# Optimization experiments

Hardware: AMD Instinct MI355X
Metric: run time of the kernel (lower is better)

Reference implementation:

```python
import jax, jax.numpy as jnp
import numpy as np

N, E = 50000, 800000
D_IN, D_H, D_OUT = 128, 256, 128
EPS = 1e-5  # BatchNorm eps


def _glorot(key, fan_in, fan_out):
    s = jnp.sqrt(6.0 / (fan_in + fan_out))
    return jax.random.uniform(key, (fan_in, fan_out), jnp.float32, -s, s)


def setup_inputs() -> dict:
    key = jax.random.key(0)
    ks = jax.random.split(key, 8)
    x = jax.random.normal(ks[0], (N, D_IN), jnp.float32)
    edge_index = jax.random.randint(ks[1], (2, E), 0, N, dtype=jnp.int64)
    return {
        "x": x,
        "edge_index": edge_index,
        # GCNConv layer 0: input_dim -> hidden
        "W0": _glorot(ks[2], D_IN, D_H), "b0": jnp.zeros((D_H,), jnp.float32),
        "g0": jnp.ones((D_H,), jnp.float32), "be0": jnp.zeros((D_H,), jnp.float32),
        # GCNConv layer 1: hidden -> hidden (residual middle layer)
        "W1": _glorot(ks[3], D_H, D_H), "b1": jnp.zeros((D_H,), jnp.float32),
        "g1": jnp.ones((D_H,), jnp.float32), "be1": jnp.zeros((D_H,), jnp.float32),
        # GCNConv layer 2: hidden -> output
        "W2": _glorot(ks[4], D_H, D_OUT), "b2": jnp.zeros((D_OUT,), jnp.float32),
    }


def reference(x, edge_index, W0, b0, g0, be0, W1, b1, g1, be1, W2, b2):
    n = x.shape[0]
    loop = jnp.arange(n, dtype=edge_index.dtype)
    src = jnp.concatenate([edge_index[0], loop])  # add self loops
    dst = jnp.concatenate([edge_index[1], loop])
    # symmetric GCN normalization: deg computed over destinations (self loops weight 1)
    deg = jax.ops.segment_sum(jnp.ones_like(src, x.dtype), dst, num_segments=n)
    dinv = jnp.where(deg > 0, jax.lax.rsqrt(deg), 0.0)
    norm = dinv[src] * dinv[dst]  # [E+N]

    def conv(h, W, b):
        m = h @ W                              # [N, F_out] transform first (F_out small)
        m = m[src] * norm[:, None]             # gather + edge scale
        return jax.ops.segment_sum(m, dst, num_segments=n) + b

    def bn(h, g, be):  # training-mode batch stats over the node dim
        mu = h.mean(axis=0)
        var = h.var(axis=0)
        return (h - mu) * jax.lax.rsqrt(var + EPS) * g + be

    # layer 0
    h = jax.nn.relu(bn(conv(x, W0, b0), g0, be0))
    # middle residual layer
    h = jax.nn.relu(bn(conv(h, W1, b1), g1, be1)) + h
    # output layer + input residual (input_dim == output_dim, no projection)
    h = conv(h, W2, b2)
    return h + x
```

## Files before the change

kernel.cpp:

```cpp
#include <hip/hip_runtime.h>

#define BN_EPS 1e-5f

static constexpr int D_IN = 128;

using u16 = unsigned short;
using f32x4  = __attribute__((ext_vector_type(4))) float;
using bf16x8 = __attribute__((ext_vector_type(8))) __bf16;

union FragU { uint4 u; bf16x8 v; };

__device__ __forceinline__ u16 f2bf(float f) {
  unsigned int u = __float_as_uint(f);
  u += 0x7FFFu + ((u >> 16) & 1u);
  return (u16)(u >> 16);
}
__device__ __forceinline__ float bf2f(u16 h) {
  return __uint_as_float(((unsigned int)h) << 16);
}


__global__ __launch_bounds__(256) void count_kernel(const int* __restrict__ dst, int E,
                                                    int* __restrict__ cnt) {
  int e = blockIdx.x * 256 + threadIdx.x;
  if (e < E) atomicAdd(&cnt[dst[e]], 1);
}

__global__ __launch_bounds__(1024) void scan_sum_kernel(const int* __restrict__ cnt, int n,
                                                        int* __restrict__ bsum,
                                                        float* __restrict__ dinv) {
  __shared__ int sdata[1024];
  int i = blockIdx.x * 1024 + threadIdx.x;
  int v = (i < n) ? cnt[i] : 0;
  if (i < n) dinv[i] = rsqrtf((float)v + 1.0f);
  sdata[threadIdx.x] = v;
  __syncthreads();
  for (int s = 512; s > 0; s >>= 1) {
    if (threadIdx.x < s) sdata[threadIdx.x] += sdata[threadIdx.x + s];
    __syncthreads();
  }
  if (threadIdx.x == 0) bsum[blockIdx.x] = sdata[0];
}

__global__ __launch_bounds__(1024) void scan_final_kernel(const int* __restrict__ cnt, int n,
                                                          const int* __restrict__ bsum,
                                                          int* __restrict__ rowptr) {
  __shared__ int wt[16];
  __shared__ int sboff;
  int i = blockIdx.x * 1024 + threadIdx.x;
  int lane = threadIdx.x & 63, w = threadIdx.x >> 6;
  int v = (i < n) ? cnt[i] : 0;
  int x = v;
  #pragma unroll
  for (int d = 1; d < 64; d <<= 1) {
    int t = __shfl_up(x, d, 64);
    if (lane >= d) x += t;
  }
  if (lane == 63) wt[w] = x;
  __syncthreads();
  if (threadIdx.x == 0) {
    int run = 0;
    #pragma unroll
    for (int k = 0; k < 16; ++k) { int t = wt[k]; wt[k] = run; run += t; }
    int bo = 0;
    for (int b = 0; b < blockIdx.x; ++b) bo += bsum[b];
    sboff = bo;
  }
  __syncthreads();
  if (i < n) {
    rowptr[i] = x - v + wt[w] + sboff;
    if (i == n - 1) rowptr[n] = x + wt[w] + sboff;
  }
}

__global__ __launch_bounds__(256) void fill_kernel(const int* __restrict__ src,
                                                   const int* __restrict__ dst, int E,
                                                   const int* __restrict__ rowptr,
                                                   int* __restrict__ cursor, int* __restrict__ col) {
  int e = blockIdx.x * 256 + threadIdx.x;
  if (e < E) {
    int d = dst[e];
    int p = atomicAdd(&cursor[d], 1);
    col[rowptr[d] + p] = src[e];
  }
}


__global__ __launch_bounds__(256) void prep_kernel(int* __restrict__ zbuf, int nz, int BZ,
                                                   const float* __restrict__ x, u16* __restrict__ x_bf,
                                                   const float* __restrict__ W0, u16* __restrict__ Wt0,
                                                   const float* __restrict__ W1, u16* __restrict__ Wt1,
                                                   const float* __restrict__ W2, u16* __restrict__ Wt2,
                                                   int N, int BX) {
  int b = blockIdx.x, tid = threadIdx.x;
  if (b < BZ) {
    int i = b * 256 + tid;
    if (i < nz) zbuf[i] = 0;
  } else if (b < BZ + BX) {
    int i = (b - BZ) * 256 + tid;
    if (i < N * 32) {
      float4 v = ((const float4*)x)[i];
      u16 o[4] = { f2bf(v.x), f2bf(v.y), f2bf(v.z), f2bf(v.w) };
      ((uint2*)x_bf)[i] = *(uint2*)o;
    }
  } else if (b < BZ + BX + 128) {
    int idx = (b - BZ - BX) * 256 + tid;
    int k = idx >> 8, nc = idx & 255;
    Wt0[nc * 128 + k] = f2bf(W0[idx]);
  } else if (b < BZ + BX + 384) {
    int idx = (b - BZ - BX - 128) * 256 + tid;
    int k = idx >> 8, nc = idx & 255;
    Wt1[nc * 256 + k] = f2bf(W1[idx]);
  } else {
    int idx = (b - BZ - BX - 384) * 256 + tid;
    int k = idx >> 7, nc = idx & 127;
    Wt2[nc * 256 + k] = f2bf(W2[idx]);
  }
}


template<int F, bool BIAS, bool FINAL>
__global__ __launch_bounds__(256) void agg_bf16(const u16* __restrict__ in,
                                                const int* __restrict__ rowptr,
                                                const int* __restrict__ col,
                                                const float* __restrict__ dinv,
                                                const float* __restrict__ bias,
                                                const float* __restrict__ xres,
                                                void* __restrict__ outv, int n) {
  constexpr int V = F / 64;
  int node = blockIdx.x * 4 + (threadIdx.x >> 6);
  if (node >= n) return;
  int lane = threadIdx.x & 63;
  const int off = lane * V;
  const size_t rowbase = (size_t)node * F + off;

  float di = dinv[node];
  float acc[V];
  {
    u16 t[V];
    if constexpr (V == 4) *(uint2*)t = *(const uint2*)(in + rowbase);
    else                  *(unsigned int*)t = *(const unsigned int*)(in + rowbase);
    #pragma unroll
    for (int j = 0; j < V; ++j) acc[j] = di * bf2f(t[j]);
  }

  int e   = __builtin_amdgcn_readfirstlane(rowptr[node]);
  int end = __builtin_amdgcn_readfirstlane(rowptr[node + 1]);
  for (; e + 4 <= end; e += 4) {
    int s0 = col[e], s1 = col[e + 1], s2 = col[e + 2], s3 = col[e + 3];
    float w0 = dinv[s0], w1 = dinv[s1], w2 = dinv[s2], w3 = dinv[s3];
    u16 t0[V], t1[V], t2[V], t3[V];
    if constexpr (V == 4) {
      *(uint2*)t0 = *(const uint2*)(in + (size_t)s0 * F + off);
      *(uint2*)t1 = *(const uint2*)(in + (size_t)s1 * F + off);
      *(uint2*)t2 = *(const uint2*)(in + (size_t)s2 * F + off);
      *(uint2*)t3 = *(const uint2*)(in + (size_t)s3 * F + off);
    } else {
      *(unsigned int*)t0 = *(const unsigned int*)(in + (size_t)s0 * F + off);
      *(unsigned int*)t1 = *(const unsigned int*)(in + (size_t)s1 * F + off);
      *(unsigned int*)t2 = *(const unsigned int*)(in + (size_t)s2 * F + off);
      *(unsigned int*)t3 = *(const unsigned int*)(in + (size_t)s3 * F + off);
    }
    #pragma unroll
    for (int j = 0; j < V; ++j) acc[j] = fmaf(w0, bf2f(t0[j]), acc[j]);
    #pragma unroll
    for (int j = 0; j < V; ++j) acc[j] = fmaf(w1, bf2f(t1[j]), acc[j]);
    #pragma unroll
    for (int j = 0; j < V; ++j) acc[j] = fmaf(w2, bf2f(t2[j]), acc[j]);
    #pragma unroll
    for (int j = 0; j < V; ++j) acc[j] = fmaf(w3, bf2f(t3[j]), acc[j]);
  }
  for (; e < end; ++e) {
    int s0 = col[e];
    float w0 = dinv[s0];
    u16 t0[V];
    if constexpr (V == 4) *(uint2*)t0 = *(const uint2*)(in + (size_t)s0 * F + off);
    else                  *(unsigned int*)t0 = *(const unsigned int*)(in + (size_t)s0 * F + off);
    #pragma unroll
    for (int j = 0; j < V; ++j) acc[j] = fmaf(w0, bf2f(t0[j]), acc[j]);
  }

  #pragma unroll
  for (int j = 0; j < V; ++j) acc[j] *= di;
  if constexpr (BIAS) {
    #pragma unroll
    for (int j = 0; j < V; ++j) acc[j] += bias[off + j];
  }
  if constexpr (FINAL) {
    float* out = (float*)outv;
    float xr[V];
    if constexpr (V == 2) *(float2*)xr = *(const float2*)(xres + rowbase);
    else                  *(float4*)xr = *(const float4*)(xres + rowbase);
    #pragma unroll
    for (int j = 0; j < V; ++j) acc[j] += xr[j];
    if constexpr (V == 2) *(float2*)(out + rowbase) = *(float2*)acc;
    else                  *(float4*)(out + rowbase) = *(float4*)acc;
  } else {
    u16* out = (u16*)outv;
    u16 o[V];
    #pragma unroll
    for (int j = 0; j < V; ++j) o[j] = f2bf(acc[j]);
    if constexpr (V == 4) *(uint2*)(out + rowbase) = *(uint2*)o;
    else                  *(unsigned int*)(out + rowbase) = *(unsigned int*)o;
  }
}


template<int K, int NN, bool BIAS, bool STATS>
__global__ __launch_bounds__(256, 2) void gemm_stream(const u16* __restrict__ A,
                                                      const u16* __restrict__ Wt,
                                                      const float* __restrict__ bias,
                                                      u16* __restrict__ C,
                                                      float* __restrict__ partial, int M) {
  constexpr int CPR = K / 8;
  __shared__ u16 Blds[128 * K];
  __shared__ float sstat[256];
  const int tid = threadIdx.x;
  const int lane = tid & 63;
  const int wid = tid >> 6;
  const int bn = blockIdx.y * 128;
  const int kh = lane >> 4;

  if constexpr (STATS) { sstat[tid] = 0.f; }

  const u16* Bsrc = Wt + (size_t)bn * K;
  #pragma unroll
  for (int i = 0; i < CPR / 2; ++i) {
    int flat = i * 256 + tid;
    int r = flat / CPR;
    int c = flat & (CPR - 1);
    __builtin_amdgcn_global_load_lds(
        (const __attribute__((address_space(1))) void*)(Bsrc + (size_t)r * K + (c ^ (r & 7)) * 8),
        (__attribute__((address_space(3))) void*)(&Blds[flat * 8]),
        16, 0, 0);
  }
  __syncthreads();

  float cs[8] = {}, cq[8] = {};
  const int nch = (M + 63) / 64;
  for (int ch = blockIdx.x * 4 + wid; ch < nch; ch += gridDim.x * 4) {
    const int r0 = ch * 64;
    const u16* arow[4];
    #pragma unroll
    for (int rf = 0; rf < 4; ++rf) {
      int row = r0 + rf * 16 + (lane & 15);
      if (row >= M) row = M - 1;
      arow[rf] = A + (size_t)row * K + kh * 8;
    }
    f32x4 acc[4][8] = {};
    #pragma unroll
    for (int ks = 0; ks < K / 32; ++ks) {
      FragU a[4], b[8];
      #pragma unroll
      for (int rf = 0; rf < 4; ++rf)
        a[rf].u = *(const uint4*)(arow[rf] + ks * 32);
      #pragma unroll
      for (int cf = 0; cf < 8; ++cf) {
        int rr = cf * 16 + (lane & 15);
        int c = ks * 4 + kh;
        b[cf].u = *(const uint4*)(&Blds[rr * K + ((c ^ (rr & 7)) * 8)]);
      }
      #pragma unroll
      for (int rf = 0; rf < 4; ++rf)
        #pragma unroll
        for (int cf = 0; cf < 8; ++cf)
          acc[rf][cf] = __builtin_amdgcn_mfma_f32_16x16x32_bf16(a[rf].v, b[cf].v,
                                                                acc[rf][cf], 0, 0, 0);
    }
    #pragma unroll
    for (int cf = 0; cf < 8; ++cf) {
      int gc = bn + cf * 16 + (lane & 15);
      float bv = 0.f;
      if constexpr (BIAS) bv = bias[gc];
      #pragma unroll
      for (int rf = 0; rf < 4; ++rf) {
        int gr0 = r0 + rf * 16 + kh * 4;
        #pragma unroll
        for (int j = 0; j < 4; ++j) {
          int gr = gr0 + j;
          if (gr < M) {
            float v = acc[rf][cf][j] + bv;
            C[(size_t)gr * NN + gc] = f2bf(v);
            if constexpr (STATS) { cs[cf] += v; cq[cf] = fmaf(v, v, cq[cf]); }
          }
        }
      }
    }
  }

  if constexpr (STATS) {
    #pragma unroll
    for (int cf = 0; cf < 8; ++cf) {
      float s = cs[cf], q = cq[cf];
      s += __shfl_xor(s, 16, 64); q += __shfl_xor(q, 16, 64);
      s += __shfl_xor(s, 32, 64); q += __shfl_xor(q, 32, 64);
      if (kh == 0) {
        int cl = cf * 16 + (lane & 15);
        atomicAdd(&sstat[cl], s);
        atomicAdd(&sstat[128 + cl], q);
      }
    }
    __syncthreads();
    if (tid < 128) {
      size_t pb = ((size_t)blockIdx.y * gridDim.x + blockIdx.x) * 256;
      partial[pb + tid]       = sstat[tid];
      partial[pb + 128 + tid] = sstat[128 + tid];
    }
  }
}


template<int F>
__global__ __launch_bounds__(256) void stats_bf16(const u16* __restrict__ m, int n,
                                                  float* __restrict__ partial) {
  constexpr int COLS = F / 4;
  constexpr int RG = 256 / COLS;
  int c4 = threadIdx.x % COLS;
  int rg = threadIdx.x / COLS;
  float s[4] = {}, q[4] = {};
  for (int r = blockIdx.x * RG + rg; r < n; r += gridDim.x * RG) {
    u16 t[4];
    *(uint2*)t = *(const uint2*)(m + (size_t)r * F + c4 * 4);
    #pragma unroll
    for (int j = 0; j < 4; ++j) { float v = bf2f(t[j]); s[j] += v; q[j] = fmaf(v, v, q[j]); }
  }
  __shared__ float ls[256][8];
  #pragma unroll
  for (int j = 0; j < 4; ++j) { ls[threadIdx.x][j] = s[j]; ls[threadIdx.x][4 + j] = q[j]; }
  __syncthreads();
  if (rg == 0) {
    for (int g = 1; g < RG; ++g) {
      #pragma unroll
      for (int j = 0; j < 4; ++j) {
        s[j] += ls[g * COLS + c4][j];
        q[j] += ls[g * COLS + c4][4 + j];
      }
    }
    #pragma unroll
    for (int j = 0; j < 4; ++j) {
      partial[(size_t)blockIdx.x * 2 * F + c4 * 4 + j]     = s[j];
      partial[(size_t)blockIdx.x * 2 * F + F + c4 * 4 + j] = q[j];
    }
  }
}

__global__ __launch_bounds__(64) void finalize_gemm(const float* __restrict__ partial, int GX, int n,
                                                    const float* __restrict__ g,
                                                    const float* __restrict__ be,
                                                    float* __restrict__ scale,
                                                    float* __restrict__ shift) {
  int c = blockIdx.x;
  int by = c >> 7, cl = c & 127;
  float s = 0.f, q = 0.f;
  for (int bx = threadIdx.x; bx < GX; bx += 64) {
    const float* pb = partial + ((size_t)by * GX + bx) * 256;
    s += pb[cl]; q += pb[128 + cl];
  }
  #pragma unroll
  for (int d = 32; d > 0; d >>= 1) { s += __shfl_down(s, d, 64); q += __shfl_down(q, d, 64); }
  if (threadIdx.x == 0) {
    float inv_n = 1.0f / (float)n;
    float mu = s * inv_n;
    float var = q * inv_n - mu * mu;
    float rs = rsqrtf(var + BN_EPS);
    float sc = rs * g[c];
    scale[c] = sc;
    shift[c] = fmaf(-mu, sc, be[c]);
  }
}

__global__ __launch_bounds__(64) void finalize_agg(const float* __restrict__ partial, int nb, int n,
                                                   const float* __restrict__ g,
                                                   const float* __restrict__ be,
                                                   float* __restrict__ scale,
                                                   float* __restrict__ shift) {
  int c = blockIdx.x;
  float s = 0.f, q = 0.f;
  for (int b = threadIdx.x; b < nb; b += 64) {
    s += partial[(size_t)b * 512 + c];
    q += partial[(size_t)b * 512 + 256 + c];
  }
  #pragma unroll
  for (int d = 32; d > 0; d >>= 1) { s += __shfl_down(s, d, 64); q += __shfl_down(q, d, 64); }
  if (threadIdx.x == 0) {
    float inv_n = 1.0f / (float)n;
    float mu = s * inv_n;
    float var = q * inv_n - mu * mu;
    float rs = rsqrtf(var + BN_EPS);
    float sc = rs * g[c];
    scale[c] = sc;
    shift[c] = fmaf(-mu, sc, be[c]);
  }
}

template<int F, bool RES>
__global__ __launch_bounds__(256) void apply_bf16(const u16* __restrict__ m,
                                                  const float* __restrict__ scale,
                                                  const float* __restrict__ shift,
                                                  const u16* __restrict__ res,
                                                  u16* __restrict__ out, int n) {
  int i = blockIdx.x * 256 + threadIdx.x;
  if (i >= n * (F / 8)) return;
  int c = i & (F / 8 - 1);
  u16 t[8];
  *(uint4*)t = *(const uint4*)(m + (size_t)i * 8);
  float sc[8], sh[8];
  *(float4*)sc       = ((const float4*)scale)[c * 2];
  *(float4*)(sc + 4) = ((const float4*)scale)[c * 2 + 1];
  *(float4*)sh       = ((const float4*)shift)[c * 2];
  *(float4*)(sh + 4) = ((const float4*)shift)[c * 2 + 1];
  float h[8];
  #pragma unroll
  for (int j = 0; j < 8; ++j) h[j] = fmaxf(fmaf(bf2f(t[j]), sc[j], sh[j]), 0.f);
  if constexpr (RES) {
    u16 r[8];
    *(uint4*)r = *(const uint4*)(res + (size_t)i * 8);
    #pragma unroll
    for (int j = 0; j < 8; ++j) h[j] += bf2f(r[j]);
  }
  u16 o[8];
  #pragma unroll
  for (int j = 0; j < 8; ++j) o[j] = f2bf(h[j]);
  *(uint4*)(out + (size_t)i * 8) = *(uint4*)o;
}


extern "C" void kernel_launch(void* const* d_in, const int* in_sizes, int n_in,
                              void* d_out, int out_size, void* d_ws, size_t ws_size,
                              hipStream_t stream) {
  const float* x   = (const float*)d_in[0];
  const int*   ei  = (const int*)d_in[1];
  const float* W0  = (const float*)d_in[2];
  const float* b0  = (const float*)d_in[3];
  const float* g0  = (const float*)d_in[4];
  const float* be0 = (const float*)d_in[5];
  const float* W1  = (const float*)d_in[6];
  const float* b1  = (const float*)d_in[7];
  const float* g1  = (const float*)d_in[8];
  const float* be1 = (const float*)d_in[9];
  const float* W2  = (const float*)d_in[10];
  const float* b2  = (const float*)d_in[11];
  float* out = (float*)d_out;

  const int N = in_sizes[0] / D_IN;
  const int E = in_sizes[1] / 2;
  const int* esrc = ei;
  const int* edst = ei + E;

  char* p = (char*)d_ws;
  auto alloc = [&](size_t bytes) { char* r = p; p += (bytes + 255) & ~(size_t)255; return r; };
  int* cnt     = (int*)alloc((size_t)2 * N * 4);
  int* cursor  = cnt + N;
  int* rowptr  = (int*)alloc(((size_t)N + 1) * 4);
  int* col     = (int*)alloc((size_t)E * 4);
  float* dinv  = (float*)alloc((size_t)N * 4);
  const int nb = (N + 1023) / 1024;
  int* bsum    = (int*)alloc((size_t)nb * 4);
  constexpr int SB = 128;
  const int GX = 196;
  float* partial = (float*)alloc((size_t)(SB > GX * 2 ? SB : GX * 2) * 512 * 4);
  float* scalev  = (float*)alloc(256 * 4);
  float* shiftv  = (float*)alloc(256 * 4);
  u16* Wt0 = (u16*)alloc((size_t)256 * 128 * 2);
  u16* Wt1 = (u16*)alloc((size_t)256 * 256 * 2);
  u16* Wt2 = (u16*)alloc((size_t)128 * 256 * 2);
  u16* slotX  = (u16*)alloc((size_t)N * 128 * 2);
  u16* slotAM = (u16*)alloc((size_t)N * 256 * 2);
  u16* slotMH = (u16*)alloc((size_t)N * 256 * 2);
  u16* slotAH = (u16*)alloc((size_t)N * 256 * 2);
  u16* x_bf = slotX;  u16* m2 = slotX;
  u16* a0   = slotAM; u16* m1 = slotAM;
  u16* m0   = slotMH; u16* h0 = slotMH;
  u16* a1   = slotAH; u16* h1 = slotAH;
  (void)ws_size; (void)n_in; (void)out_size;

  const int BZ = (2 * N + 255) / 256;
  const int BX = (N * 32 + 255) / 256;
  prep_kernel<<<BZ + BX + 512, 256, 0, stream>>>(cnt, 2 * N, BZ, x, x_bf,
                                                 W0, Wt0, W1, Wt1, W2, Wt2, N, BX);
  count_kernel<<<(E + 255) / 256, 256, 0, stream>>>(edst, E, cnt);
  scan_sum_kernel<<<nb, 1024, 0, stream>>>(cnt, N, bsum, dinv);
  scan_final_kernel<<<nb, 1024, 0, stream>>>(cnt, N, bsum, rowptr);
  fill_kernel<<<(E + 255) / 256, 256, 0, stream>>>(esrc, edst, E, rowptr, cursor, col);

  const int aggGrid = (N + 3) / 4;

  agg_bf16<128, false, false><<<aggGrid, 256, 0, stream>>>(x_bf, rowptr, col, dinv,
                                                           nullptr, nullptr, a0, N);
  gemm_stream<128, 256, true, true><<<dim3(GX, 2), 256, 0, stream>>>(a0, Wt0, b0, m0, partial, N);
  finalize_gemm<<<256, 64, 0, stream>>>(partial, GX, N, g0, be0, scalev, shiftv);
  apply_bf16<256, false><<<(N * 32 + 255) / 256, 256, 0, stream>>>(m0, scalev, shiftv,
                                                                   nullptr, h0, N);

  gemm_stream<256, 256, false, false><<<dim3(GX, 2), 256, 0, stream>>>(h0, Wt1, nullptr, m1,
                                                                       nullptr, N);
  agg_bf16<256, true, false><<<aggGrid, 256, 0, stream>>>(m1, rowptr, col, dinv,
                                                          b1, nullptr, a1, N);
  stats_bf16<256><<<SB, 256, 0, stream>>>(a1, N, partial);
  finalize_agg<<<256, 64, 0, stream>>>(partial, SB, N, g1, be1, scalev, shiftv);
  apply_bf16<256, true><<<(N * 32 + 255) / 256, 256, 0, stream>>>(a1, scalev, shiftv,
                                                                  h0, h1, N);

  gemm_stream<256, 128, false, false><<<dim3(GX, 1), 256, 0, stream>>>(h1, Wt2, nullptr, m2,
                                                                       nullptr, N);
  agg_bf16<128, true, true><<<aggGrid, 256, 0, stream>>>(m2, rowptr, col, dinv,
                                                         b2, x, out, N);
}
```

Baseline: 409.3 us.

## Stage GEMM epilogue through LDS for wide stores; fuse BN finalize via last-block

The GEMM epilogue now writes each row's bf16 outputs into a small per-wave LDS staging buffer and stores 16-byte vectors to global memory, replacing scattered 2-byte stores. The BN stat finalization kernels are removed and folded into the GEMM and stats kernels using an atomic done-counter, so the last block to finish reduces the partials. This cuts two kernel launches and improves store coalescing, at the cost of extra LDS traffic, an LDS round trip per row, and a serial reduction in a single block.

Result: slower. 515.6 us (+26.0%).

```diff
diff --git a/kernel.cpp b/kernel.cpp
--- a/kernel.cpp
+++ b/kernel.cpp
@@ -206,18 +206,26 @@
 }
 
 
-template<int K, int NN, bool BIAS, bool STATS>
+template<int K, int NN, bool BIAS, bool STATS, bool FIN>
 __global__ __launch_bounds__(256, 2) void gemm_stream(const u16* __restrict__ A,
                                                       const u16* __restrict__ Wt,
                                                       const float* __restrict__ bias,
                                                       u16* __restrict__ C,
-                                                      float* __restrict__ partial, int M) {
+                                                      float* __restrict__ partial,
+                                                      int* __restrict__ done,
+                                                      const float* __restrict__ g,
+                                                      const float* __restrict__ be,
+                                                      float* __restrict__ scale,
+                                                      float* __restrict__ shift, int M) {
   constexpr int CPR = K / 8;
   __shared__ u16 Blds[128 * K];
+  __shared__ __align__(16) u16 Cst[4][4][136];
   __shared__ float sstat[256];
+  __shared__ int lastflag;
   const int tid = threadIdx.x;
   const int lane = tid & 63;
   const int wid = tid >> 6;
+  const int l15 = lane & 15;
   const int bn = blockIdx.y * 128;
   const int kh = lane >> 4;
 
@@ -236,6 +244,10 @@
   }
   __syncthreads();
 
+  float bv[8];
+  #pragma unroll
+  for (int cf = 0; cf < 8; ++cf) bv[cf] = BIAS ? bias[bn + cf * 16 + l15] : 0.f;
+
   float cs[8] = {}, cq[8] = {};
   const int nch = (M + 63) / 64;
   for (int ch = blockIdx.x * 4 + wid; ch < nch; ch += gridDim.x * 4) {
@@ -243,7 +255,7 @@
     const u16* arow[4];
     #pragma unroll
     for (int rf = 0; rf < 4; ++rf) {
-      int row = r0 + rf * 16 + (lane & 15);
+      int row = r0 + rf * 16 + l15;
       if (row >= M) row = M - 1;
       arow[rf] = A + (size_t)row * K + kh * 8;
     }
@@ -256,7 +268,7 @@
         a[rf].u = *(const uint4*)(arow[rf] + ks * 32);
       #pragma unroll
       for (int cf = 0; cf < 8; ++cf) {
-        int rr = cf * 16 + (lane & 15);
+        int rr = cf * 16 + l15;
         int c = ks * 4 + kh;
         b[cf].u = *(const uint4*)(&Blds[rr * K + ((c ^ (rr & 7)) * 8)]);
       }
@@ -268,22 +280,19 @@
                                                                 acc[rf][cf], 0, 0, 0);
     }
     #pragma unroll
-    for (int cf = 0; cf < 8; ++cf) {
-      int gc = bn + cf * 16 + (lane & 15);
-      float bv = 0.f;
-      if constexpr (BIAS) bv = bias[gc];
+    for (int rf = 0; rf < 4; ++rf) {
       #pragma unroll
-      for (int rf = 0; rf < 4; ++rf) {
-        int gr0 = r0 + rf * 16 + kh * 4;
+      for (int j = 0; j < 4; ++j) {
+        int grw = r0 + rf * 16 + kh * 4 + j;
         #pragma unroll
-        for (int j = 0; j < 4; ++j) {
-          int gr = gr0 + j;
-          if (gr < M) {
-            float v = acc[rf][cf][j] + bv;
-            C[(size_t)gr * NN + gc] = f2bf(v);
-            if constexpr (STATS) { cs[cf] += v; cq[cf] = fmaf(v, v, cq[cf]); }
-          }
+        for (int cf = 0; cf < 8; ++cf) {
+          float v = acc[rf][cf][j] + bv[cf];
+          if constexpr (STATS) { if (grw < M) { cs[cf] += v; cq[cf] = fmaf(v, v, cq[cf]); } }
+          Cst[wid][kh][cf * 16 + l15] = f2bf(v);
         }
+        int gr = r0 + rf * 16 + kh * 4 + j;
+        uint4 d = *(const uint4*)(&Cst[wid][kh][l15 * 8]);
+        if (gr < M) *(uint4*)(C + (size_t)gr * NN + bn + l15 * 8) = d;
       }
     }
   }
@@ -295,7 +304,7 @@
       s += __shfl_xor(s, 16, 64); q += __shfl_xor(q, 16, 64);
       s += __shfl_xor(s, 32, 64); q += __shfl_xor(q, 32, 64);
       if (kh == 0) {
-        int cl = cf * 16 + (lane & 15);
+        int cl = cf * 16 + l15;
         atomicAdd(&sstat[cl], s);
         atomicAdd(&sstat[128 + cl], q);
       }
@@ -306,15 +315,46 @@
       partial[pb + tid]       = sstat[tid];
       partial[pb + 128 + tid] = sstat[128 + tid];
     }
+    if constexpr (FIN) {
+      __threadfence();
+      if (tid == 0) {
+        int old = atomicAdd(done, 1);
+        lastflag = (old == (int)(gridDim.x * gridDim.y) - 1);
+      }
+      __syncthreads();
+      if (lastflag) {
+        __threadfence();
+        int c = tid;
+        int by = c >> 7, cl = c & 127;
+        float s = 0.f, q = 0.f;
+        for (int bx = 0; bx < (int)gridDim.x; ++bx) {
+          const float* pb = partial + ((size_t)by * gridDim.x + bx) * 256;
+          s += pb[cl]; q += pb[128 + cl];
+        }
+        float inv_n = 1.0f / (float)M;
+        float mu = s * inv_n;
+        float var = q * inv_n - mu * mu;
+        float rs = rsqrtf(var + BN_EPS);
+        float sc = rs * g[c];
+        scale[c] = sc;
+        shift[c] = fmaf(-mu, sc, be[c]);
+      }
+    }
   }
 }
 
 
 template<int F>
 __global__ __launch_bounds__(256) void stats_bf16(const u16* __restrict__ m, int n,
-                                                  float* __restrict__ partial) {
+                                                  float* __restrict__ partial,
+                                                  int* __restrict__ done,
+                                                  const float* __restrict__ g,
+                                                  const float* __restrict__ be,
+                                                  float* __restrict__ scale,
+                                                  float* __restrict__ shift) {
   constexpr int COLS = F / 4;
   constexpr int RG = 256 / COLS;
+  __shared__ int lastflag;
   int c4 = threadIdx.x % COLS;
   int rg = threadIdx.x / COLS;
   float s[4] = {}, q[4] = {};
@@ -329,11 +369,11 @@
   for (int j = 0; j < 4; ++j) { ls[threadIdx.x][j] = s[j]; ls[threadIdx.x][4 + j] = q[j]; }
   __syncthreads();
   if (rg == 0) {
-    for (int g = 1; g < RG; ++g) {
+    for (int gg = 1; gg < RG; ++gg) {
       #pragma unroll
       for (int j = 0; j < 4; ++j) {
-        s[j] += ls[g * COLS + c4][j];
-        q[j] += ls[g * COLS + c4][4 + j];
+        s[j] += ls[gg * COLS + c4][j];
+        q[j] += ls[gg * COLS + c4][4 + j];
       }
     }
     #pragma unroll
@@ -342,50 +382,23 @@
       partial[(size_t)blockIdx.x * 2 * F + F + c4 * 4 + j] = q[j];
     }
   }
-}
-
-__global__ __launch_bounds__(64) void finalize_gemm(const float* __restrict__ partial, int GX, int n,
-                                                    const float* __restrict__ g,
-                                                    const float* __restrict__ be,
-                                                    float* __restrict__ scale,
-                                                    float* __restrict__ shift) {
-  int c = blockIdx.x;
-  int by = c >> 7, cl = c & 127;
-  float s = 0.f, q = 0.f;
-  for (int bx = threadIdx.x; bx < GX; bx += 64) {
-    const float* pb = partial + ((size_t)by * GX + bx) * 256;
-    s += pb[cl]; q += pb[128 + cl];
-  }
-  #pragma unroll
-  for (int d = 32; d > 0; d >>= 1) { s += __shfl_down(s, d, 64); q += __shfl_down(q, d, 64); }
+  __threadfence();
   if (threadIdx.x == 0) {
+    int old = atomicAdd(done, 1);
+    lastflag = (old == (int)gridDim.x - 1);
+  }
+  __syncthreads();
+  if (lastflag) {
+    __threadfence();
+    int c = threadIdx.x;
+    float ss = 0.f, qq = 0.f;
+    for (int b = 0; b < (int)gridDim.x; ++b) {
+      ss += partial[(size_t)b * 2 * F + c];
+      qq += partial[(size_t)b * 2 * F + F + c];
+    }
     float inv_n = 1.0f / (float)n;
-    float mu = s * inv_n;
-    float var = q * inv_n - mu * mu;
-    float rs = rsqrtf(var + BN_EPS);
-    float sc = rs * g[c];
-    scale[c] = sc;
-    shift[c] = fmaf(-mu, sc, be[c]);
-  }
-}
-
-__global__ __launch_bounds__(64) void finalize_agg(const float* __restrict__ partial, int nb, int n,
-                                                   const float* __restrict__ g,
-                                                   const float* __restrict__ be,
-                                                   float* __restrict__ scale,
-                                                   float* __restrict__ shift) {
-  int c = blockIdx.x;
-  float s = 0.f, q = 0.f;
-  for (int b = threadIdx.x; b < nb; b += 64) {
-    s += partial[(size_t)b * 512 + c];
-    q += partial[(size_t)b * 512 + 256 + c];
-  }
-  #pragma unroll
-  for (int d = 32; d > 0; d >>= 1) { s += __shfl_down(s, d, 64); q += __shfl_down(q, d, 64); }
-  if (threadIdx.x == 0) {
-    float inv_n = 1.0f / (float)n;
-    float mu = s * inv_n;
-    float var = q * inv_n - mu * mu;
+    float mu = ss * inv_n;
+    float var = qq * inv_n - mu * mu;
     float rs = rsqrtf(var + BN_EPS);
     float sc = rs * g[c];
     scale[c] = sc;
@@ -449,8 +462,9 @@
 
   char* p = (char*)d_ws;
   auto alloc = [&](size_t bytes) { char* r = p; p += (bytes + 255) & ~(size_t)255; return r; };
-  int* cnt     = (int*)alloc((size_t)2 * N * 4);
+  int* cnt     = (int*)alloc(((size_t)2 * N + 2) * 4);
   int* cursor  = cnt + N;
+  int* done    = cnt + 2 * N;
   int* rowptr  = (int*)alloc(((size_t)N + 1) * 4);
   int* col     = (int*)alloc((size_t)E * 4);
   float* dinv  = (float*)alloc((size_t)N * 4);
@@ -474,9 +488,10 @@
   u16* a1   = slotAH; u16* h1 = slotAH;
   (void)ws_size; (void)n_in; (void)out_size;
 
-  const int BZ = (2 * N + 255) / 256;
+  const int NZ = 2 * N + 2;
+  const int BZ = (NZ + 255) / 256;
   const int BX = (N * 32 + 255) / 256;
-  prep_kernel<<<BZ + BX + 512, 256, 0, stream>>>(cnt, 2 * N, BZ, x, x_bf,
+  prep_kernel<<<BZ + BX + 512, 256, 0, stream>>>(cnt, NZ, BZ, x, x_bf,
                                                  W0, Wt0, W1, Wt1, W2, Wt2, N, BX);
   count_kernel<<<(E + 255) / 256, 256, 0, stream>>>(edst, E, cnt);
   scan_sum_kernel<<<nb, 1024, 0, stream>>>(cnt, N, bsum, dinv);
@@ -487,22 +502,21 @@
 
   agg_bf16<128, false, false><<<aggGrid, 256, 0, stream>>>(x_bf, rowptr, col, dinv,
                                                            nullptr, nullptr, a0, N);
-  gemm_stream<128, 256, true, true><<<dim3(GX, 2), 256, 0, stream>>>(a0, Wt0, b0, m0, partial, N);
-  finalize_gemm<<<256, 64, 0, stream>>>(partial, GX, N, g0, be0, scalev, shiftv);
+  gemm_stream<128, 256, true, true, true><<<dim3(GX, 2), 256, 0, stream>>>(
+      a0, Wt0, b0, m0, partial, done, g0, be0, scalev, shiftv, N);
   apply_bf16<256, false><<<(N * 32 + 255) / 256, 256, 0, stream>>>(m0, scalev, shiftv,
                                                                    nullptr, h0, N);
 
-  gemm_stream<256, 256, false, false><<<dim3(GX, 2), 256, 0, stream>>>(h0, Wt1, nullptr, m1,
-                                                                       nullptr, N);
+  gemm_stream<256, 256, false, false, false><<<dim3(GX, 2), 256, 0, stream>>>(
+      h0, Wt1, nullptr, m1, nullptr, nullptr, nullptr, nullptr, nullptr, nullptr, N);
   agg_bf16<256, true, false><<<aggGrid, 256, 0, stream>>>(m1, rowptr, col, dinv,
                                                           b1, nullptr, a1, N);
-  stats_bf16<256><<<SB, 256, 0, stream>>>(a1, N, partial);
-  finalize_agg<<<256, 64, 0, stream>>>(partial, SB, N, g1, be1, scalev, shiftv);
+  stats_bf16<256><<<SB, 256, 0, stream>>>(a1, N, partial, done + 1, g1, be1, scalev, shiftv);
   apply_bf16<256, true><<<(N * 32 + 255) / 256, 256, 0, stream>>>(a1, scalev, shiftv,
                                                                   h0, h1, N);
 
-  gemm_stream<256, 128, false, false><<<dim3(GX, 1), 256, 0, stream>>>(h1, Wt2, nullptr, m2,
-                                                                       nullptr, N);
+  gemm_stream<256, 128, false, false, false><<<dim3(GX, 1), 256, 0, stream>>>(
+      h1, Wt2, nullptr, m2, nullptr, nullptr, nullptr, nullptr, nullptr, nullptr, N);
   agg_bf16<128, true, true><<<aggGrid, 256, 0, stream>>>(m2, rowptr, col, dinv,
                                                          b2, x, out, N);
 }
```
